# Optimization experiments

Measured on AMD Instinct MI355X. Metric: run time of the kernel, lower is better.

## Reference

```python
import jax, jax.numpy as jnp
import numpy as np

WH, WW = 8, 8            # window_size
NUM_HEADS = 8
DIM = 256
CPB_HIDDEN = 512
N = WH * WW


def _make_coords_table():
    # [1, 2*WH-1, 2*WW-1, 2] log-spaced continuous relative coords (Swin-V2)
    h = np.arange(-(WH - 1), WH, dtype=np.float32)
    w = np.arange(-(WW - 1), WW, dtype=np.float32)
    gh, gw = np.meshgrid(h, w, indexing='ij')
    table = np.stack([gh, gw], axis=-1)[None]  # [1,2WH-1,2WW-1,2]
    table[..., 0] /= (WH - 1)
    table[..., 1] /= (WW - 1)
    table *= 8.0
    table = np.sign(table) * np.log2(np.abs(table) + 1.0) / np.log2(8.0)
    return jnp.asarray(table, dtype=jnp.float32)


def _make_rel_pos_index():
    ch = np.arange(WH)
    cw = np.arange(WW)
    coords = np.stack(np.meshgrid(ch, cw, indexing='ij'))   # [2,WH,WW]
    cf = coords.reshape(2, -1)                               # [2,N]
    rel = cf[:, :, None] - cf[:, None, :]                    # [2,N,N]
    rel = rel.transpose(1, 2, 0).astype(np.int32)            # [N,N,2]
    rel[..., 0] += WH - 1
    rel[..., 1] += WW - 1
    rel[..., 0] *= 2 * WW - 1
    return jnp.asarray(rel.sum(-1), dtype=jnp.int32)         # [N,N]


def setup_inputs() -> dict:
    key = jax.random.key(0)
    ks = jax.random.split(key, 8)
    B_ = 2048
    nW = 64
    x = jax.random.normal(ks[0], (B_, N, DIM), dtype=jnp.float32)
    mask = jnp.zeros((nW, N, N), dtype=jnp.float32)
    qkv_w = jax.random.normal(ks[1], (3 * DIM, DIM), dtype=jnp.float32) * 0.02
    q_bias = jnp.zeros((DIM,), dtype=jnp.float32)
    v_bias = jnp.zeros((DIM,), dtype=jnp.float32)
    logit_scale = jnp.log(10.0 * jnp.ones((NUM_HEADS, 1, 1), dtype=jnp.float32))
    cpb_w1 = jax.random.normal(ks[2], (CPB_HIDDEN, 2), dtype=jnp.float32) * 0.02
    cpb_b1 = jnp.zeros((CPB_HIDDEN,), dtype=jnp.float32)
    cpb_w2 = jax.random.normal(ks[3], (NUM_HEADS, CPB_HIDDEN), dtype=jnp.float32) * 0.02
    proj_w = jax.random.normal(ks[4], (DIM, DIM), dtype=jnp.float32) * 0.02
    proj_b = jnp.zeros((DIM,), dtype=jnp.float32)
    return {
        'x': x, 'mask': mask,
        'qkv_w': qkv_w, 'q_bias': q_bias, 'v_bias': v_bias,
        'logit_scale': logit_scale,
        'cpb_w1': cpb_w1, 'cpb_b1': cpb_b1, 'cpb_w2': cpb_w2,
        'proj_w': proj_w, 'proj_b': proj_b,
        'coords_table': _make_coords_table(),
        'rel_idx': _make_rel_pos_index(),
    }


def reference(x, mask, qkv_w, q_bias, v_bias, logit_scale,
              cpb_w1, cpb_b1, cpb_w2, proj_w, proj_b,
              coords_table, rel_idx):
    B_, n, C = x.shape
    H = NUM_HEADS
    hd = C // H

    # qkv with [q_bias, 0, v_bias]
    qkv_bias = jnp.concatenate([q_bias, jnp.zeros_like(v_bias), v_bias])
    qkv = x @ qkv_w.T + qkv_bias                         # [B,N,3C]
    qkv = qkv.reshape(B_, n, 3, H, hd).transpose(2, 0, 3, 1, 4)
    q, k, v = qkv[0], qkv[1], qkv[2]                     # [B,H,N,hd]

    # cosine attention: L2-normalized q,k (eps as in F.normalize)
    qn = q / jnp.maximum(jnp.linalg.norm(q, axis=-1, keepdims=True), 1e-12)
    kn = k / jnp.maximum(jnp.linalg.norm(k, axis=-1, keepdims=True), 1e-12)
    attn = jnp.einsum('bhnd,bhmd->bhnm', qn, kn)         # [B,H,N,N]

    max_log = jnp.log(jnp.asarray(1.0 / 0.01, dtype=x.dtype))
    scale = jnp.exp(jnp.minimum(logit_scale, max_log))   # [H,1,1]
    attn = attn * scale

    # MLP relative position bias: 2 -> 512 -> H, gather, 16*sigmoid
    hid = jax.nn.relu(coords_table @ cpb_w1.T + cpb_b1)  # [1,2WH-1,2WW-1,512]
    table = (hid @ cpb_w2.T).reshape(-1, H)              # [(2WH-1)(2WW-1), H]
    bias = table[rel_idx.reshape(-1)].reshape(n, n, H)
    bias = 16.0 * jax.nn.sigmoid(bias.transpose(2, 0, 1))  # [H,N,N]
    attn = attn + bias[None]

    nW = mask.shape[0]
    attn = attn.reshape(B_ // nW, nW, H, n, n) + mask[None, :, None]
    attn = attn.reshape(B_, H, n, n)
    attn = jax.nn.softmax(attn, axis=-1)

    out = jnp.einsum('bhnm,bhmd->bhnd', attn, v)         # [B,H,N,hd]
    out = out.transpose(0, 2, 1, 3).reshape(B_, n, C)
    return out @ proj_w.T + proj_b
```

## Files before the change

### kernel.cpp

```cpp
#include <hip/hip_runtime.h>
#include <hip/hip_bf16.h>

typedef unsigned short u16;
typedef unsigned int   u32;
typedef __attribute__((ext_vector_type(8))) short short8;
typedef __attribute__((ext_vector_type(4))) short short4v;
typedef __attribute__((ext_vector_type(4))) float f32x4;

__device__ __forceinline__ u16 f2bf(float f) {
  u32 u = __float_as_uint(f);
  u32 r = (u + 0x7fffu + ((u >> 16) & 1u)) >> 16;
  return (u16)r;
}

__global__ __launch_bounds__(256) void wcvt_kernel(
    const float* __restrict__ qkvw, const float* __restrict__ pw,
    u16* __restrict__ wq, u16* __restrict__ wp) {
  const int e = (blockIdx.x * 256 + threadIdx.x) * 4;
  if (e < 196608) {
    const float4 v = *(const float4*)(qkvw + e);
    short4v o; o[0]=(short)f2bf(v.x); o[1]=(short)f2bf(v.y);
    o[2]=(short)f2bf(v.z); o[3]=(short)f2bf(v.w);
    *(short4v*)(wq + e) = o;
  } else {
    const int e2 = e - 196608;
    const float4 v = *(const float4*)(pw + e2);
    short4v o; o[0]=(short)f2bf(v.x); o[1]=(short)f2bf(v.y);
    o[2]=(short)f2bf(v.z); o[3]=(short)f2bf(v.w);
    *(short4v*)(wp + e2) = o;
  }
}

__global__ __launch_bounds__(256) void cpb_kernel(
    const float* __restrict__ ct, const float* __restrict__ w1,
    const float* __restrict__ b1, const float* __restrict__ w2,
    float* __restrict__ table) {
  const int r = blockIdx.x;
  const int t = threadIdx.x;
  const int lane = t & 63, wave = t >> 6;
  const float c0 = ct[r * 2 + 0];
  const float c1 = ct[r * 2 + 1];
  float acc[8] = {0.f, 0.f, 0.f, 0.f, 0.f, 0.f, 0.f, 0.f};
  for (int j = t; j < 512; j += 256) {
    float hid = fmaxf(c0 * w1[j * 2] + c1 * w1[j * 2 + 1] + b1[j], 0.f);
#pragma unroll
    for (int hh = 0; hh < 8; ++hh) acc[hh] += hid * w2[hh * 512 + j];
  }
#pragma unroll
  for (int hh = 0; hh < 8; ++hh)
#pragma unroll
    for (int off = 1; off < 64; off <<= 1) acc[hh] += __shfl_xor(acc[hh], off);
  __shared__ float red[4][8];
  if (lane == 0)
#pragma unroll
    for (int hh = 0; hh < 8; ++hh) red[wave][hh] = acc[hh];
  __syncthreads();
  if (t < 8) table[r * 8 + t] = red[0][t] + red[1][t] + red[2][t] + red[3][t];
}

__global__ __launch_bounds__(256) void gather_kernel(
    const float* __restrict__ table, const int* __restrict__ rel,
    float* __restrict__ bias16) {
  const int e = blockIdx.x * 256 + threadIdx.x;
  const int hh = e >> 12, ij = e & 4095;
  const float v = table[rel[ij] * 8 + hh];
  bias16[e] = 16.f * (1.f / (1.f + __expf(-v)));
}

__global__ __launch_bounds__(512) void fused_kernel(
    const float* __restrict__ X,
    const float* __restrict__ mask,
    const float* __restrict__ bias16,
    const float* __restrict__ lsc,
    const u16*  __restrict__ Wqb,
    const float* __restrict__ qb, const float* __restrict__ vbias,
    const u16*  __restrict__ Wpb,
    const float* __restrict__ pb,
    float* __restrict__ out) {
  __shared__ __attribute__((aligned(16))) u16 sA[16896];
  __shared__ __attribute__((aligned(16))) u16 sB[36864];
  __shared__ __attribute__((aligned(16))) u16 sV[18432];

  const int bw = blockIdx.x;
  const int w  = bw & 63;
  const int tid  = threadIdx.x;
  const int wave = tid >> 6, lane = tid & 63;
  const int l15 = lane & 15, l4 = lane >> 4;

  {
    const int cq  = tid & 7;
    const int rlo = tid >> 3;
    const float* xrow = X + ((size_t)bw * 64 + rlo) * 256;
#pragma unroll
    for (int kf = 0; kf < 8; ++kf) {
      const float4 xv = *(const float4*)(xrow + kf * 32 + cq * 4);
      short4v t4; t4[0]=(short)f2bf(xv.x); t4[1]=(short)f2bf(xv.y);
      t4[2]=(short)f2bf(xv.z); t4[3]=(short)f2bf(xv.w);
      *(short4v*)&sA[kf * 2048 + rlo * 32 + cq * 4] = t4;
    }
  }
  __syncthreads();

  {
    f32x4 acc[4][6];
#pragma unroll
    for (int mi = 0; mi < 4; ++mi)
#pragma unroll
      for (int nj = 0; nj < 6; ++nj) acc[mi][nj] = (f32x4){0.f, 0.f, 0.f, 0.f};

#pragma unroll
    for (int kf = 0; kf < 8; ++kf) {
      short8 af[4];
#pragma unroll
      for (int mi = 0; mi < 4; ++mi)
        af[mi] = *(const short8*)&sA[kf * 2048 + (mi * 16 + l15) * 32 + l4 * 8];
#pragma unroll
      for (int nj = 0; nj < 6; ++nj) {
        const short8 bf = *(const short8*)(
            Wqb + (size_t)(wave * 96 + nj * 16 + l15) * 256 + kf * 32 + l4 * 8);
#pragma unroll
        for (int mi = 0; mi < 4; ++mi)
          acc[mi][nj] = __builtin_amdgcn_mfma_f32_16x16x32_bf16(af[mi], bf, acc[mi][nj], 0, 0, 0);
      }
    }

#pragma unroll
    for (int t = 0; t < 3; ++t) {
      const int nbase = wave * 96 + t * 32;
      const int which = nbase >> 8;
      const int h = (nbase >> 5) & 7;
      const int c = nbase & 255;
      if (which <= 1) {
        u16* dst = (which == 0 ? sB : sB + 16384) + h * 2048;
        const float b0 = (which == 0) ? qb[c + l15] : 0.f;
        const float b1 = (which == 0) ? qb[c + 16 + l15] : 0.f;
#pragma unroll
        for (int mi = 0; mi < 4; ++mi)
#pragma unroll
          for (int r = 0; r < 4; ++r) {
            const float v0 = acc[mi][2 * t][r] + b0;
            const float v1 = acc[mi][2 * t + 1][r] + b1;
            float ss = v0 * v0 + v1 * v1;
            ss += __shfl_xor(ss, 1); ss += __shfl_xor(ss, 2);
            ss += __shfl_xor(ss, 4); ss += __shfl_xor(ss, 8);
            const float inv = 1.f / fmaxf(sqrtf(ss), 1e-12f);
            const int m = mi * 16 + l4 * 4 + r;
            dst[m * 32 + l15]      = f2bf(v0 * inv);
            dst[m * 32 + 16 + l15] = f2bf(v1 * inv);
          }
      } else {
        const float b0 = vbias[c + l15];
        const float b1 = vbias[c + 16 + l15];
        u16* dst = sV + h * 2304;
#pragma unroll
        for (int mi = 0; mi < 4; ++mi)
#pragma unroll
          for (int r = 0; r < 4; ++r) {
            const int m = mi * 16 + l4 * 4 + r;
            dst[l15 * 72 + m]        = f2bf(acc[mi][2 * t][r] + b0);
            dst[(16 + l15) * 72 + m] = f2bf(acc[mi][2 * t + 1][r] + b1);
          }
      }
    }
  }
  __syncthreads();

  {
    const int h = wave;
    short8 aq[4], bk[4];
#pragma unroll
    for (int i = 0; i < 4; ++i)
      aq[i] = *(const short8*)&sB[h * 2048 + (i * 16 + l15) * 32 + l4 * 8];
#pragma unroll
    for (int j = 0; j < 4; ++j)
      bk[j] = *(const short8*)&sB[16384 + h * 2048 + (j * 16 + l15) * 32 + l4 * 8];

    f32x4 s[4][4];
#pragma unroll
    for (int i = 0; i < 4; ++i)
#pragma unroll
      for (int j = 0; j < 4; ++j) {
        const f32x4 z = {0.f, 0.f, 0.f, 0.f};
        s[i][j] = __builtin_amdgcn_mfma_f32_16x16x32_bf16(aq[i], bk[j], z, 0, 0, 0);
      }
    __syncthreads();

    const float scale = expf(fminf(lsc[h], 4.60517018598809136804f));
    const float* brow = bias16 + h * 4096;
    const float* mrow = mask + (size_t)w * 4096;
    u16* pW = sB + wave * 4608;

#pragma unroll
    for (int i = 0; i < 4; ++i)
#pragma unroll
      for (int r = 0; r < 4; ++r) {
        const int m = i * 16 + l4 * 4 + r;
        float v0[4]; float mx = -3.0e38f;
#pragma unroll
        for (int j = 0; j < 4; ++j) {
          const int col = j * 16 + l15;
          const float sv = s[i][j][r] * scale + brow[m * 64 + col] + mrow[m * 64 + col];
          v0[j] = sv; mx = fmaxf(mx, sv);
        }
        mx = fmaxf(mx, __shfl_xor(mx, 1)); mx = fmaxf(mx, __shfl_xor(mx, 2));
        mx = fmaxf(mx, __shfl_xor(mx, 4)); mx = fmaxf(mx, __shfl_xor(mx, 8));
        float sum = 0.f;
#pragma unroll
        for (int j = 0; j < 4; ++j) { v0[j] = __expf(v0[j] - mx); sum += v0[j]; }
        sum += __shfl_xor(sum, 1); sum += __shfl_xor(sum, 2);
        sum += __shfl_xor(sum, 4); sum += __shfl_xor(sum, 8);
        const float isum = 1.f / sum;
#pragma unroll
        for (int j = 0; j < 4; ++j)
          pW[m * 72 + j * 16 + l15] = f2bf(v0[j] * isum);
      }

    f32x4 oa[4][2];
#pragma unroll
    for (int i = 0; i < 4; ++i)
#pragma unroll
      for (int nb = 0; nb < 2; ++nb) oa[i][nb] = (f32x4){0.f, 0.f, 0.f, 0.f};
#pragma unroll
    for (int kb = 0; kb < 2; ++kb) {
      short8 pa[4];
#pragma unroll
      for (int i = 0; i < 4; ++i)
        pa[i] = *(const short8*)&pW[(i * 16 + l15) * 72 + kb * 32 + l4 * 8];
#pragma unroll
      for (int nb = 0; nb < 2; ++nb) {
        const short8 vb8 = *(const short8*)&sV[h * 2304 + (nb * 16 + l15) * 72 + kb * 32 + l4 * 8];
#pragma unroll
        for (int i = 0; i < 4; ++i)
          oa[i][nb] = __builtin_amdgcn_mfma_f32_16x16x32_bf16(pa[i], vb8, oa[i][nb], 0, 0, 0);
      }
    }
#pragma unroll
    for (int i = 0; i < 4; ++i)
#pragma unroll
      for (int nb = 0; nb < 2; ++nb)
#pragma unroll
        for (int r = 0; r < 4; ++r) {
          const int m = i * 16 + l4 * 4 + r;
          sA[m * 264 + h * 32 + nb * 16 + l15] = f2bf(oa[i][nb][r]);
        }
  }
  __syncthreads();

  {
    const int n0 = wave * 32;
    f32x4 pacc[4][2];
#pragma unroll
    for (int mi = 0; mi < 4; ++mi)
#pragma unroll
      for (int nj = 0; nj < 2; ++nj) pacc[mi][nj] = (f32x4){0.f, 0.f, 0.f, 0.f};
#pragma unroll
    for (int k0 = 0; k0 < 256; k0 += 32) {
      short8 afr[4];
#pragma unroll
      for (int mi = 0; mi < 4; ++mi)
        afr[mi] = *(const short8*)&sA[(mi * 16 + l15) * 264 + k0 + l4 * 8];
#pragma unroll
      for (int nj = 0; nj < 2; ++nj) {
        const short8 bfr = *(const short8*)(
            Wpb + (size_t)(n0 + nj * 16 + l15) * 256 + k0 + l4 * 8);
#pragma unroll
        for (int mi = 0; mi < 4; ++mi)
          pacc[mi][nj] = __builtin_amdgcn_mfma_f32_16x16x32_bf16(afr[mi], bfr, pacc[mi][nj], 0, 0, 0);
      }
    }
    float* orow = out + (size_t)bw * 64 * 256;
#pragma unroll
    for (int mi = 0; mi < 4; ++mi)
#pragma unroll
      for (int nj = 0; nj < 2; ++nj) {
        const int n = n0 + nj * 16 + l15;
        const float bias = pb[n];
#pragma unroll
        for (int r = 0; r < 4; ++r) {
          const int m = mi * 16 + l4 * 4 + r;
          orow[(size_t)m * 256 + n] = pacc[mi][nj][r] + bias;
        }
      }
  }
}

extern "C" void kernel_launch(void* const* d_in, const int* in_sizes, int n_in,
                              void* d_out, int out_size, void* d_ws, size_t ws_size,
                              hipStream_t stream) {
  (void)in_sizes; (void)n_in; (void)out_size; (void)ws_size;
  const float* x    = (const float*)d_in[0];
  const float* mask = (const float*)d_in[1];
  const float* qkvw = (const float*)d_in[2];
  const float* qb   = (const float*)d_in[3];
  const float* vb   = (const float*)d_in[4];
  const float* lsc  = (const float*)d_in[5];
  const float* w1   = (const float*)d_in[6];
  const float* b1   = (const float*)d_in[7];
  const float* w2   = (const float*)d_in[8];
  const float* pw   = (const float*)d_in[9];
  const float* pb   = (const float*)d_in[10];
  const float* ct   = (const float*)d_in[11];
  const int* rel    = (const int*)d_in[12];
  float* out = (float*)d_out;

  char* ws = (char*)d_ws;
  float* table  = (float*)(ws);
  float* bias16 = (float*)(ws + 16384);
  u16* Wqb = (u16*)(ws + 262144);
  u16* Wpb = (u16*)(ws + 720896);

  wcvt_kernel<<<256, 256, 0, stream>>>(qkvw, pw, Wqb, Wpb);
  cpb_kernel<<<225, 256, 0, stream>>>(ct, w1, b1, w2, table);
  gather_kernel<<<128, 256, 0, stream>>>(table, rel, bias16);
  fused_kernel<<<2048, 512, 0, stream>>>(x, mask, bias16, lsc, Wqb, qb, vb,
                                         Wpb, pb, out);
}
```

Baseline: 503.2 us.

## Double fused kernel to 1024 threads and prefuse bias with mask per window

The fused attention kernel now launches 16 waves per block instead of 8, splitting each GEMM and each head's attention rows between two waves so every wave holds half the accumulators. A new pre-kernel combines the sigmoid position bias with the window mask into one per-window, per-head table, so the fused kernel does one bias load per score instead of two. This lowers register pressure per wave and raises the number of waves available to hide latency. In exchange it adds a 8 MB precomputed bias-plus-mask buffer that must be written once and then read from global or L2, and an unused bf2f helper is added.

```diff
diff --git a/kernel.cpp b/kernel.cpp
--- a/kernel.cpp
+++ b/kernel.cpp
@@ -11,6 +11,9 @@
   u32 u = __float_as_uint(f);
   u32 r = (u + 0x7fffu + ((u >> 16) & 1u)) >> 16;
   return (u16)r;
+}
+__device__ __forceinline__ float bf2f(u16 u) {
+  union { u32 i; float f; } v; v.i = ((u32)u) << 16; return v.f;
 }
 
 __global__ __launch_bounds__(256) void wcvt_kernel(
@@ -58,19 +61,25 @@
   if (t < 8) table[r * 8 + t] = red[0][t] + red[1][t] + red[2][t] + red[3][t];
 }
 
-__global__ __launch_bounds__(256) void gather_kernel(
+__global__ __launch_bounds__(256) void bm_kernel(
     const float* __restrict__ table, const int* __restrict__ rel,
-    float* __restrict__ bias16) {
-  const int e = blockIdx.x * 256 + threadIdx.x;
-  const int hh = e >> 12, ij = e & 4095;
-  const float v = table[rel[ij] * 8 + hh];
-  bias16[e] = 16.f * (1.f / (1.f + __expf(-v)));
-}
-
-__global__ __launch_bounds__(512) void fused_kernel(
+    const float* __restrict__ mask, float* __restrict__ bm) {
+  const int g = blockIdx.x * 256 + threadIdx.x;
+  const int w = g >> 13;
+  const int h = (g >> 10) & 7;
+  const int ij = (g & 1023) * 4;
+  const float4 mv = *(const float4*)(mask + (size_t)w * 4096 + ij);
+  float4 o;
+  o.x = 16.f / (1.f + __expf(-table[rel[ij + 0] * 8 + h])) + mv.x;
+  o.y = 16.f / (1.f + __expf(-table[rel[ij + 1] * 8 + h])) + mv.y;
+  o.z = 16.f / (1.f + __expf(-table[rel[ij + 2] * 8 + h])) + mv.z;
+  o.w = 16.f / (1.f + __expf(-table[rel[ij + 3] * 8 + h])) + mv.w;
+  *(float4*)(bm + ((size_t)(w * 8 + h)) * 4096 + ij) = o;
+}
+
+__global__ __launch_bounds__(1024) void fused_kernel(
     const float* __restrict__ X,
-    const float* __restrict__ mask,
-    const float* __restrict__ bias16,
+    const float* __restrict__ bm,
     const float* __restrict__ lsc,
     const u16*  __restrict__ Wqb,
     const float* __restrict__ qb, const float* __restrict__ vbias,
@@ -88,45 +97,49 @@
   const int l15 = lane & 15, l4 = lane >> 4;
 
   {
-    const int cq  = tid & 7;
-    const int rlo = tid >> 3;
-    const float* xrow = X + ((size_t)bw * 64 + rlo) * 256;
-#pragma unroll
-    for (int kf = 0; kf < 8; ++kf) {
-      const float4 xv = *(const float4*)(xrow + kf * 32 + cq * 4);
+    const int row = tid >> 4;
+    const int c4  = tid & 15;
+    const float* xrow = X + ((size_t)bw * 64 + row) * 256;
+#pragma unroll
+    for (int u = 0; u < 4; ++u) {
+      const int col = u * 64 + c4 * 4;
+      const int kf = col >> 5, co = col & 31;
+      const float4 xv = *(const float4*)(xrow + col);
       short4v t4; t4[0]=(short)f2bf(xv.x); t4[1]=(short)f2bf(xv.y);
       t4[2]=(short)f2bf(xv.z); t4[3]=(short)f2bf(xv.w);
-      *(short4v*)&sA[kf * 2048 + rlo * 32 + cq * 4] = t4;
+      *(short4v*)&sA[kf * 2048 + row * 32 + co] = t4;
     }
   }
   __syncthreads();
 
   {
-    f32x4 acc[4][6];
-#pragma unroll
-    for (int mi = 0; mi < 4; ++mi)
+    const int wm = wave & 1;
+    const int wn = wave >> 1;
+    f32x4 acc[2][6];
+#pragma unroll
+    for (int mi = 0; mi < 2; ++mi)
 #pragma unroll
       for (int nj = 0; nj < 6; ++nj) acc[mi][nj] = (f32x4){0.f, 0.f, 0.f, 0.f};
 
 #pragma unroll
     for (int kf = 0; kf < 8; ++kf) {
-      short8 af[4];
-#pragma unroll
-      for (int mi = 0; mi < 4; ++mi)
-        af[mi] = *(const short8*)&sA[kf * 2048 + (mi * 16 + l15) * 32 + l4 * 8];
+      short8 af[2];
+#pragma unroll
+      for (int mi = 0; mi < 2; ++mi)
+        af[mi] = *(const short8*)&sA[kf * 2048 + (wm * 32 + mi * 16 + l15) * 32 + l4 * 8];
 #pragma unroll
       for (int nj = 0; nj < 6; ++nj) {
         const short8 bf = *(const short8*)(
-            Wqb + (size_t)(wave * 96 + nj * 16 + l15) * 256 + kf * 32 + l4 * 8);
-#pragma unroll
-        for (int mi = 0; mi < 4; ++mi)
+            Wqb + (size_t)(wn * 96 + nj * 16 + l15) * 256 + kf * 32 + l4 * 8);
+#pragma unroll
+        for (int mi = 0; mi < 2; ++mi)
           acc[mi][nj] = __builtin_amdgcn_mfma_f32_16x16x32_bf16(af[mi], bf, acc[mi][nj], 0, 0, 0);
       }
     }
 
 #pragma unroll
     for (int t = 0; t < 3; ++t) {
-      const int nbase = wave * 96 + t * 32;
+      const int nbase = wn * 96 + t * 32;
       const int which = nbase >> 8;
       const int h = (nbase >> 5) & 7;
       const int c = nbase & 255;
@@ -135,7 +148,7 @@
         const float b0 = (which == 0) ? qb[c + l15] : 0.f;
         const float b1 = (which == 0) ? qb[c + 16 + l15] : 0.f;
 #pragma unroll
-        for (int mi = 0; mi < 4; ++mi)
+        for (int mi = 0; mi < 2; ++mi)
 #pragma unroll
           for (int r = 0; r < 4; ++r) {
             const float v0 = acc[mi][2 * t][r] + b0;
@@ -144,7 +157,7 @@
             ss += __shfl_xor(ss, 1); ss += __shfl_xor(ss, 2);
             ss += __shfl_xor(ss, 4); ss += __shfl_xor(ss, 8);
             const float inv = 1.f / fmaxf(sqrtf(ss), 1e-12f);
-            const int m = mi * 16 + l4 * 4 + r;
+            const int m = wm * 32 + mi * 16 + l4 * 4 + r;
             dst[m * 32 + l15]      = f2bf(v0 * inv);
             dst[m * 32 + 16 + l15] = f2bf(v1 * inv);
           }
@@ -153,10 +166,10 @@
         const float b1 = vbias[c + 16 + l15];
         u16* dst = sV + h * 2304;
 #pragma unroll
-        for (int mi = 0; mi < 4; ++mi)
+        for (int mi = 0; mi < 2; ++mi)
 #pragma unroll
           for (int r = 0; r < 4; ++r) {
-            const int m = mi * 16 + l4 * 4 + r;
+            const int m = wm * 32 + mi * 16 + l4 * 4 + r;
             dst[l15 * 72 + m]        = f2bf(acc[mi][2 * t][r] + b0);
             dst[(16 + l15) * 72 + m] = f2bf(acc[mi][2 * t + 1][r] + b1);
           }
@@ -166,18 +179,19 @@
   __syncthreads();
 
   {
-    const int h = wave;
-    short8 aq[4], bk[4];
-#pragma unroll
-    for (int i = 0; i < 4; ++i)
-      aq[i] = *(const short8*)&sB[h * 2048 + (i * 16 + l15) * 32 + l4 * 8];
+    const int h  = wave >> 1;
+    const int rh = wave & 1;
+    short8 aq[2], bk[4];
+#pragma unroll
+    for (int i = 0; i < 2; ++i)
+      aq[i] = *(const short8*)&sB[h * 2048 + (rh * 32 + i * 16 + l15) * 32 + l4 * 8];
 #pragma unroll
     for (int j = 0; j < 4; ++j)
       bk[j] = *(const short8*)&sB[16384 + h * 2048 + (j * 16 + l15) * 32 + l4 * 8];
 
-    f32x4 s[4][4];
-#pragma unroll
-    for (int i = 0; i < 4; ++i)
+    f32x4 s[2][4];
+#pragma unroll
+    for (int i = 0; i < 2; ++i)
 #pragma unroll
       for (int j = 0; j < 4; ++j) {
         const f32x4 z = {0.f, 0.f, 0.f, 0.f};
@@ -186,20 +200,20 @@
     __syncthreads();
 
     const float scale = expf(fminf(lsc[h], 4.60517018598809136804f));
-    const float* brow = bias16 + h * 4096;
-    const float* mrow = mask + (size_t)w * 4096;
-    u16* pW = sB + wave * 4608;
-
-#pragma unroll
-    for (int i = 0; i < 4; ++i)
+    const float* bmrow = bm + ((size_t)(w * 8 + h)) * 4096;
+    u16* pW = sB + wave * 2304;
+
+#pragma unroll
+    for (int i = 0; i < 2; ++i)
 #pragma unroll
       for (int r = 0; r < 4; ++r) {
-        const int m = i * 16 + l4 * 4 + r;
+        const int ml = i * 16 + l4 * 4 + r;
+        const int m  = rh * 32 + ml;
         float v0[4]; float mx = -3.0e38f;
 #pragma unroll
         for (int j = 0; j < 4; ++j) {
           const int col = j * 16 + l15;
-          const float sv = s[i][j][r] * scale + brow[m * 64 + col] + mrow[m * 64 + col];
+          const float sv = s[i][j][r] * scale + bmrow[m * 64 + col];
           v0[j] = sv; mx = fmaxf(mx, sv);
         }
         mx = fmaxf(mx, __shfl_xor(mx, 1)); mx = fmaxf(mx, __shfl_xor(mx, 2));
@@ -212,72 +226,73 @@
         const float isum = 1.f / sum;
 #pragma unroll
         for (int j = 0; j < 4; ++j)
-          pW[m * 72 + j * 16 + l15] = f2bf(v0[j] * isum);
-      }
-
-    f32x4 oa[4][2];
-#pragma unroll
-    for (int i = 0; i < 4; ++i)
+          pW[ml * 72 + j * 16 + l15] = f2bf(v0[j] * isum);
+      }
+
+    f32x4 oa[2][2];
+#pragma unroll
+    for (int i = 0; i < 2; ++i)
 #pragma unroll
       for (int nb = 0; nb < 2; ++nb) oa[i][nb] = (f32x4){0.f, 0.f, 0.f, 0.f};
 #pragma unroll
     for (int kb = 0; kb < 2; ++kb) {
-      short8 pa[4];
-#pragma unroll
-      for (int i = 0; i < 4; ++i)
+      short8 pa[2];
+#pragma unroll
+      for (int i = 0; i < 2; ++i)
         pa[i] = *(const short8*)&pW[(i * 16 + l15) * 72 + kb * 32 + l4 * 8];
 #pragma unroll
       for (int nb = 0; nb < 2; ++nb) {
         const short8 vb8 = *(const short8*)&sV[h * 2304 + (nb * 16 + l15) * 72 + kb * 32 + l4 * 8];
 #pragma unroll
-        for (int i = 0; i < 4; ++i)
+        for (int i = 0; i < 2; ++i)
           oa[i][nb] = __builtin_amdgcn_mfma_f32_16x16x32_bf16(pa[i], vb8, oa[i][nb], 0, 0, 0);
       }
     }
 #pragma unroll
-    for (int i = 0; i < 4; ++i)
+    for (int i = 0; i < 2; ++i)
 #pragma unroll
       for (int nb = 0; nb < 2; ++nb)
 #pragma unroll
         for (int r = 0; r < 4; ++r) {
-          const int m = i * 16 + l4 * 4 + r;
+          const int m = rh * 32 + i * 16 + l4 * 4 + r;
           sA[m * 264 + h * 32 + nb * 16 + l15] = f2bf(oa[i][nb][r]);
         }
   }
   __syncthreads();
 
   {
-    const int n0 = wave * 32;
-    f32x4 pacc[4][2];
-#pragma unroll
-    for (int mi = 0; mi < 4; ++mi)
+    const int wm = wave & 1;
+    const int n0 = (wave >> 1) * 32;
+    f32x4 pacc[2][2];
+#pragma unroll
+    for (int mi = 0; mi < 2; ++mi)
 #pragma unroll
       for (int nj = 0; nj < 2; ++nj) pacc[mi][nj] = (f32x4){0.f, 0.f, 0.f, 0.f};
 #pragma unroll
     for (int k0 = 0; k0 < 256; k0 += 32) {
-      short8 afr[4];
-#pragma unroll
-      for (int mi = 0; mi < 4; ++mi)
-        afr[mi] = *(const short8*)&sA[(mi * 16 + l15) * 264 + k0 + l4 * 8];
+      short8 afr[2];
+#pragma unroll
+      for (int mi = 0; mi < 2; ++mi)
+        afr[mi] = *(const short8*)&sA[(wm * 32 + mi * 16 + l15) * 264 + k0 + l4 * 8];
 #pragma unroll
       for (int nj = 0; nj < 2; ++nj) {
         const short8 bfr = *(const short8*)(
             Wpb + (size_t)(n0 + nj * 16 + l15) * 256 + k0 + l4 * 8);
 #pragma unroll
-        for (int mi = 0; mi < 4; ++mi)
+        for (int mi = 0; mi < 2; ++mi)
           pacc[mi][nj] = __builtin_amdgcn_mfma_f32_16x16x32_bf16(afr[mi], bfr, pacc[mi][nj], 0, 0, 0);
       }
     }
     float* orow = out + (size_t)bw * 64 * 256;
 #pragma unroll
-    for (int mi = 0; mi < 4; ++mi)
+    for (int mi = 0; mi < 2; ++mi)
 #pragma unroll
       for (int nj = 0; nj < 2; ++nj) {
         const int n = n0 + nj * 16 + l15;
         const float bias = pb[n];
 #pragma unroll
         for (int r = 0; r < 4; ++r) {
-          const int m = mi * 16 + l4 * 4 + r;
+          const int m = wm * 32 + mi * 16 + l4 * 4 + r;
           orow[(size_t)m * 256 + n] = pacc[mi][nj][r] + bias;
         }
       }
@@ -304,14 +319,14 @@
   float* out = (float*)d_out;
 
   char* ws = (char*)d_ws;
-  float* table  = (float*)(ws);
-  float* bias16 = (float*)(ws + 16384);
+  float* table = (float*)(ws);
   u16* Wqb = (u16*)(ws + 262144);
   u16* Wpb = (u16*)(ws + 720896);
+  float* bm = (float*)(ws + (1 << 20));
 
   wcvt_kernel<<<256, 256, 0, stream>>>(qkvw, pw, Wqb, Wpb);
   cpb_kernel<<<225, 256, 0, stream>>>(ct, w1, b1, w2, table);
-  gather_kernel<<<128, 256, 0, stream>>>(table, rel, bias16);
-  fused_kernel<<<2048, 512, 0, stream>>>(x, mask, bias16, lsc, Wqb, qb, vb,
-                                         Wpb, pb, out);
-}
+  bm_kernel<<<2048, 256, 0, stream>>>(table, rel, mask, bm);
+  fused_kernel<<<2048, 1024, 0, stream>>>(x, bm, lsc, Wqb, qb, vb,
+                                          Wpb, pb, out);
+}
```

After: 559.8 us. 11.3% more time.

## Precombine bias+mask per window, prefetch B fragments, raise occupancy hint

Applied to the files above, without the earlier changes.

The attention-bias gather kernel is replaced by a kernel that adds the sigmoid bias and the mask into one per-window, per-head tensor laid out for float4 loads. The fused kernel then reads that tensor with vector loads issued before the QK MFMAs, so each score needs one load instead of two scalar loads. The QKV and projection GEMM loops now software-prefetch the next k-slice of weight fragments from global memory. Launch bounds request 2 blocks per SM, which may cap registers per thread. The precombined tensor (64 windows × 8 heads × 4096 floats, 8MB) adds a pre-pass and extra workspace traffic.

```diff
diff --git a/kernel.cpp b/kernel.cpp
--- a/kernel.cpp
+++ b/kernel.cpp
@@ -58,19 +58,27 @@
   if (t < 8) table[r * 8 + t] = red[0][t] + red[1][t] + red[2][t] + red[3][t];
 }
 
-__global__ __launch_bounds__(256) void gather_kernel(
+__global__ __launch_bounds__(256) void bm_kernel(
     const float* __restrict__ table, const int* __restrict__ rel,
-    float* __restrict__ bias16) {
-  const int e = blockIdx.x * 256 + threadIdx.x;
-  const int hh = e >> 12, ij = e & 4095;
-  const float v = table[rel[ij] * 8 + hh];
-  bias16[e] = 16.f * (1.f / (1.f + __expf(-v)));
-}
-
-__global__ __launch_bounds__(512) void fused_kernel(
+    const float* __restrict__ mask, float* __restrict__ bmP) {
+  const int g = blockIdx.x * 256 + threadIdx.x;
+  const int w = g >> 13;
+  const int h = (g >> 10) & 7;
+  const int m = (g >> 4) & 63;
+  const int l = g & 15;
+  float4 o;
+#pragma unroll
+  for (int j = 0; j < 4; ++j) {
+    const int c = j * 16 + l;
+    const float t = table[rel[m * 64 + c] * 8 + h];
+    o[j] = 16.f / (1.f + __expf(-t)) + mask[(size_t)w * 4096 + m * 64 + c];
+  }
+  *(float4*)(bmP + ((((size_t)w * 8 + h) * 64 + m) * 64 + l * 4)) = o;
+}
+
+__global__ __launch_bounds__(512, 2) void fused_kernel(
     const float* __restrict__ X,
-    const float* __restrict__ mask,
-    const float* __restrict__ bias16,
+    const float* __restrict__ bmP,
     const float* __restrict__ lsc,
     const u16*  __restrict__ Wqb,
     const float* __restrict__ qb, const float* __restrict__ vbias,
@@ -102,11 +110,17 @@
   __syncthreads();
 
   {
+    const u16* wbase = Wqb + (size_t)(wave * 96 + l15) * 256 + l4 * 8;
     f32x4 acc[4][6];
 #pragma unroll
     for (int mi = 0; mi < 4; ++mi)
 #pragma unroll
       for (int nj = 0; nj < 6; ++nj) acc[mi][nj] = (f32x4){0.f, 0.f, 0.f, 0.f};
+
+    short8 bf_cur[6];
+#pragma unroll
+    for (int nj = 0; nj < 6; ++nj)
+      bf_cur[nj] = *(const short8*)(wbase + (size_t)(nj * 16) * 256);
 
 #pragma unroll
     for (int kf = 0; kf < 8; ++kf) {
@@ -114,13 +128,20 @@
 #pragma unroll
       for (int mi = 0; mi < 4; ++mi)
         af[mi] = *(const short8*)&sA[kf * 2048 + (mi * 16 + l15) * 32 + l4 * 8];
-#pragma unroll
-      for (int nj = 0; nj < 6; ++nj) {
-        const short8 bf = *(const short8*)(
-            Wqb + (size_t)(wave * 96 + nj * 16 + l15) * 256 + kf * 32 + l4 * 8);
+      short8 bf_nxt[6];
+      if (kf < 7) {
+#pragma unroll
+        for (int nj = 0; nj < 6; ++nj)
+          bf_nxt[nj] = *(const short8*)(wbase + (size_t)(nj * 16) * 256 + (kf + 1) * 32);
+      }
+#pragma unroll
+      for (int nj = 0; nj < 6; ++nj)
 #pragma unroll
         for (int mi = 0; mi < 4; ++mi)
-          acc[mi][nj] = __builtin_amdgcn_mfma_f32_16x16x32_bf16(af[mi], bf, acc[mi][nj], 0, 0, 0);
+          acc[mi][nj] = __builtin_amdgcn_mfma_f32_16x16x32_bf16(af[mi], bf_cur[nj], acc[mi][nj], 0, 0, 0);
+      if (kf < 7) {
+#pragma unroll
+        for (int nj = 0; nj < 6; ++nj) bf_cur[nj] = bf_nxt[nj];
       }
     }
 
@@ -167,6 +188,16 @@
 
   {
     const int h = wave;
+    const float* bmbase = bmP + (((size_t)(w * 8 + h)) * 64) * 64 + l15 * 4;
+    float4 bmv[4][4];
+#pragma unroll
+    for (int i = 0; i < 4; ++i)
+#pragma unroll
+      for (int r = 0; r < 4; ++r) {
+        const int m = i * 16 + l4 * 4 + r;
+        bmv[i][r] = *(const float4*)(bmbase + (size_t)m * 64);
+      }
+
     short8 aq[4], bk[4];
 #pragma unroll
     for (int i = 0; i < 4; ++i)
@@ -186,8 +217,6 @@
     __syncthreads();
 
     const float scale = expf(fminf(lsc[h], 4.60517018598809136804f));
-    const float* brow = bias16 + h * 4096;
-    const float* mrow = mask + (size_t)w * 4096;
     u16* pW = sB + wave * 4608;
 
 #pragma unroll
@@ -198,8 +227,7 @@
         float v0[4]; float mx = -3.0e38f;
 #pragma unroll
         for (int j = 0; j < 4; ++j) {
-          const int col = j * 16 + l15;
-          const float sv = s[i][j][r] * scale + brow[m * 64 + col] + mrow[m * 64 + col];
+          const float sv = s[i][j][r] * scale + bmv[i][r][j];
           v0[j] = sv; mx = fmaxf(mx, sv);
         }
         mx = fmaxf(mx, __shfl_xor(mx, 1)); mx = fmaxf(mx, __shfl_xor(mx, 2));
@@ -248,24 +276,39 @@
 
   {
     const int n0 = wave * 32;
+    const u16* pbase = Wpb + (size_t)(n0 + l15) * 256 + l4 * 8;
     f32x4 pacc[4][2];
 #pragma unroll
     for (int mi = 0; mi < 4; ++mi)
 #pragma unroll
       for (int nj = 0; nj < 2; ++nj) pacc[mi][nj] = (f32x4){0.f, 0.f, 0.f, 0.f};
-#pragma unroll
-    for (int k0 = 0; k0 < 256; k0 += 32) {
+
+    short8 bfr_cur[2];
+#pragma unroll
+    for (int nj = 0; nj < 2; ++nj)
+      bfr_cur[nj] = *(const short8*)(pbase + (size_t)(nj * 16) * 256);
+
+#pragma unroll
+    for (int ks = 0; ks < 8; ++ks) {
+      const int k0 = ks * 32;
       short8 afr[4];
 #pragma unroll
       for (int mi = 0; mi < 4; ++mi)
         afr[mi] = *(const short8*)&sA[(mi * 16 + l15) * 264 + k0 + l4 * 8];
-#pragma unroll
-      for (int nj = 0; nj < 2; ++nj) {
-        const short8 bfr = *(const short8*)(
-            Wpb + (size_t)(n0 + nj * 16 + l15) * 256 + k0 + l4 * 8);
+      short8 bfr_nxt[2];
+      if (ks < 7) {
+#pragma unroll
+        for (int nj = 0; nj < 2; ++nj)
+          bfr_nxt[nj] = *(const short8*)(pbase + (size_t)(nj * 16) * 256 + k0 + 32);
+      }
+#pragma unroll
+      for (int nj = 0; nj < 2; ++nj)
 #pragma unroll
         for (int mi = 0; mi < 4; ++mi)
-          pacc[mi][nj] = __builtin_amdgcn_mfma_f32_16x16x32_bf16(afr[mi], bfr, pacc[mi][nj], 0, 0, 0);
+          pacc[mi][nj] = __builtin_amdgcn_mfma_f32_16x16x32_bf16(afr[mi], bfr_cur[nj], pacc[mi][nj], 0, 0, 0);
+      if (ks < 7) {
+#pragma unroll
+        for (int nj = 0; nj < 2; ++nj) bfr_cur[nj] = bfr_nxt[nj];
       }
     }
     float* orow = out + (size_t)bw * 64 * 256;
@@ -304,14 +347,14 @@
   float* out = (float*)d_out;
 
   char* ws = (char*)d_ws;
-  float* table  = (float*)(ws);
-  float* bias16 = (float*)(ws + 16384);
+  float* table = (float*)(ws);
   u16* Wqb = (u16*)(ws + 262144);
   u16* Wpb = (u16*)(ws + 720896);
+  float* bmP = (float*)(ws + (1 << 20));
 
   wcvt_kernel<<<256, 256, 0, stream>>>(qkvw, pw, Wqb, Wpb);
   cpb_kernel<<<225, 256, 0, stream>>>(ct, w1, b1, w2, table);
-  gather_kernel<<<128, 256, 0, stream>>>(table, rel, bias16);
-  fused_kernel<<<2048, 512, 0, stream>>>(x, mask, bias16, lsc, Wqb, qb, vb,
+  bm_kernel<<<2048, 256, 0, stream>>>(table, rel, mask, bmP);
+  fused_kernel<<<2048, 512, 0, stream>>>(x, bmP, lsc, Wqb, qb, vb,
                                          Wpb, pb, out);
 }
```

New measurement: 498.6 us. No clear change (-0.9%).
